# Optimization experiments

Hardware: AMD Instinct MI355X
Metric: run time of the kernel (lower is better)

The kernel has to match this reference:

```python
import jax, jax.numpy as jnp
import numpy as np

N_NODES = 20000
N_EDGES = 320000
N_FEAT = 128
HID = 64
HEADS = 4
N_CLS = 16
NEG_SLOPE = 0.2


def setup_inputs() -> dict:
    key = jax.random.key(0)
    ks = jax.random.split(key, 12)
    x = jax.random.normal(ks[0], (N_NODES, N_FEAT), dtype=jnp.float32)
    edge_index = jax.random.randint(ks[1], (2, N_EDGES), 0, N_NODES, dtype=jnp.int64)
    # layer 1: GATConv(128 -> 64, heads=4, concat)
    s1 = 1.0 / np.sqrt(N_FEAT)
    W1 = jax.random.uniform(ks[2], (N_FEAT, HEADS * HID), jnp.float32, -s1, s1)
    a_src1 = jax.random.uniform(ks[3], (HEADS, HID), jnp.float32, -s1, s1)
    a_dst1 = jax.random.uniform(ks[4], (HEADS, HID), jnp.float32, -s1, s1)
    b1 = jnp.zeros((HEADS * HID,), jnp.float32)
    # layer 2: GATConv(256 -> 16, heads=1)
    s2 = 1.0 / np.sqrt(HEADS * HID)
    W2 = jax.random.uniform(ks[5], (HEADS * HID, N_CLS), jnp.float32, -s2, s2)
    a_src2 = jax.random.uniform(ks[6], (1, N_CLS), jnp.float32, -s2, s2)
    a_dst2 = jax.random.uniform(ks[7], (1, N_CLS), jnp.float32, -s2, s2)
    b2 = jnp.zeros((N_CLS,), jnp.float32)
    return {"x": x, "edge_index": edge_index, "W1": W1, "a_src1": a_src1,
            "a_dst1": a_dst1, "b1": b1, "W2": W2, "a_src2": a_src2,
            "a_dst2": a_dst2, "b2": b2}


def gat_conv(x, src, dst, W, a_src, a_dst, bias, n_nodes):
    # x: [N, F_in]; W: [F_in, H*C]; a_src/a_dst: [H, C]
    H, C = a_src.shape
    h = (x @ W).reshape(n_nodes, H, C)                     # [N, H, C]
    al_src = jnp.sum(h * a_src[None], axis=-1)             # [N, H]
    al_dst = jnp.sum(h * a_dst[None], axis=-1)             # [N, H]
    e = jax.nn.leaky_relu(al_src[src] + al_dst[dst], NEG_SLOPE)  # [E, H]
    # segment softmax over incoming edges of each destination node
    m = jax.ops.segment_max(e, dst, num_segments=n_nodes)  # [N, H]
    e = jnp.exp(e - m[dst])
    denom = jax.ops.segment_sum(e, dst, num_segments=n_nodes)
    alpha = e / (denom[dst] + 1e-16)                       # [E, H]
    msg = h[src] * alpha[:, :, None]                       # [E, H, C]
    out = jax.ops.segment_sum(msg, dst, num_segments=n_nodes)  # [N, H, C]
    return out.reshape(n_nodes, H * C) + bias


def reference(x, edge_index, W1, a_src1, a_dst1, b1, W2, a_src2, a_dst2, b2):
    n = x.shape[0]
    loops = jnp.arange(n, dtype=edge_index.dtype)
    src = jnp.concatenate([edge_index[0], loops])
    dst = jnp.concatenate([edge_index[1], loops])
    # eval mode: dropout is identity
    h = jax.nn.elu(gat_conv(x, src, dst, W1, a_src1, a_dst1, b1, n))
    out = gat_conv(h, src, dst, W2, a_src2, a_dst2, b2, n)
    return out
```

## Files before the change

### kernel.cpp

```cpp
#include <hip/hip_runtime.h>
#include <hip/hip_bf16.h>
#include <hip/hip_fp16.h>
#include <math.h>

#define N_NODES 20000
#define N_EDGES 320000
#define E_TOT   (N_EDGES + N_NODES)
#define N_FEAT  128
#define NEG_SLOPE 0.2f
#define MAXDEG  96

typedef _Float16 half8 __attribute__((ext_vector_type(8)));
typedef float f32x4 __attribute__((ext_vector_type(4)));

__global__ void k_zero(int* __restrict__ cur){
  int i = blockIdx.x * blockDim.x + threadIdx.x;
  if (i < N_NODES) cur[i] = 0;
}

__global__ void k_pre(const int* __restrict__ ei, int* __restrict__ cur,
                      int* __restrict__ adjS,
                      const float* __restrict__ x, _Float16* __restrict__ xh,
                      const float* __restrict__ W1, _Float16* __restrict__ W1t){
  int tid = blockIdx.x * blockDim.x + threadIdx.x;
  if (tid < E_TOT){
    int s, d;
    if (tid < N_EDGES){ s = ei[tid]; d = ei[N_EDGES + tid]; }
    else              { s = d = tid - N_EDGES; }
    int pos = atomicAdd(&cur[d], 1);
    if (pos < MAXDEG) adjS[d * MAXDEG + pos] = s;
  }
  if (tid < (N_NODES * N_FEAT / 8)){
    float4 a = *(const float4*)&x[(size_t)tid * 8];
    float4 b = *(const float4*)&x[(size_t)tid * 8 + 4];
    union { __half2 h2[4]; half8 h8; } u;
    u.h2[0] = __floats2half2_rn(a.x, a.y);
    u.h2[1] = __floats2half2_rn(a.z, a.w);
    u.h2[2] = __floats2half2_rn(b.x, b.y);
    u.h2[3] = __floats2half2_rn(b.z, b.w);
    *(half8*)&xh[(size_t)tid * 8] = u.h8;
  }
  int u2 = tid - (N_NODES * N_FEAT / 8);
  if (u2 >= 0 && u2 < 4096){
    int n = u2 >> 4, ks = u2 & 15;
    union { __half2 h2[4]; half8 h8; } u;
    float v[8];
    #pragma unroll
    for (int r = 0; r < 8; ++r) v[r] = W1[(size_t)(ks * 8 + r) * 256 + n];
    u.h2[0] = __floats2half2_rn(v[0], v[1]);
    u.h2[1] = __floats2half2_rn(v[2], v[3]);
    u.h2[2] = __floats2half2_rn(v[4], v[5]);
    u.h2[3] = __floats2half2_rn(v[6], v[7]);
    *(half8*)&W1t[(size_t)n * 128 + ks * 8] = u.h8;
  }
}

__global__ __launch_bounds__(256) void k_gemm1(
                        const _Float16* __restrict__ xh, const _Float16* __restrict__ W1t,
                        const float* __restrict__ as1, const float* __restrict__ ad1,
                        _Float16* __restrict__ h1h,
                        float* __restrict__ alS, float* __restrict__ alD){
  __shared__ _Float16 xt[64][136];
  __shared__ _Float16 Wt[64][136];
  int t  = threadIdx.x;
  int m0 = blockIdx.x * 64;
  int by = blockIdx.y;
  int j0 = by * 64;
  #pragma unroll
  for (int ii = 0; ii < 4; ++ii){
    int f = t + ii * 256;
    int r = f >> 4, s = f & 15;
    half8 xv = (half8)(_Float16)0.f;
    if (m0 + r < N_NODES) xv = *(const half8*)&xh[(size_t)(m0 + r) * 128 + s * 8];
    *(half8*)&xt[r][s * 8] = xv;
    half8 wv = *(const half8*)&W1t[(size_t)(j0 + r) * 128 + s * 8];
    *(half8*)&Wt[r][s * 8] = wv;
  }
  __syncthreads();

  int w = t >> 6, lane = t & 63;
  int g = lane >> 4, mi = lane & 15;
  f32x4 acc[4] = {};
  #pragma unroll
  for (int kk = 0; kk < 4; ++kk){
    int ko = kk * 32 + g * 8;
    half8 b = *(const half8*)&xt[w * 16 + mi][ko];
    #pragma unroll
    for (int s = 0; s < 4; ++s){
      half8 a = *(const half8*)&Wt[s * 16 + mi][ko];
      acc[s] = __builtin_amdgcn_mfma_f32_16x16x32_f16(a, b, acc[s], 0, 0, 0);
    }
  }

  int m = m0 + w * 16 + mi;
  float s_ = 0.f, d_ = 0.f;
  #pragma unroll
  for (int s = 0; s < 4; ++s){
    int nb = j0 + s * 16 + g * 4;
    float4 asv = *(const float4*)&as1[nb];
    float4 adv = *(const float4*)&ad1[nb];
    s_ += acc[s][0] * asv.x + acc[s][1] * asv.y + acc[s][2] * asv.z + acc[s][3] * asv.w;
    d_ += acc[s][0] * adv.x + acc[s][1] * adv.y + acc[s][2] * adv.z + acc[s][3] * adv.w;
    if (m < N_NODES){
      union { __half2 h2[2]; float2 f2; } u;
      u.h2[0] = __floats2half2_rn(acc[s][0], acc[s][1]);
      u.h2[1] = __floats2half2_rn(acc[s][2], acc[s][3]);
      *(float2*)&h1h[(size_t)m * 256 + nb] = u.f2;
    }
  }
  s_ += __shfl_xor(s_, 16); s_ += __shfl_xor(s_, 32);
  d_ += __shfl_xor(d_, 16); d_ += __shfl_xor(d_, 32);
  if (g == 0 && m < N_NODES){ alS[m * 4 + by] = s_; alD[m * 4 + by] = d_; }
}

__global__ __launch_bounds__(256) void k_attn1(
                        const int* __restrict__ cur, const int* __restrict__ adjS,
                        const __half* __restrict__ h1h,
                        const float* __restrict__ alS, const float* __restrict__ alD,
                        const float* __restrict__ b1, _Float16* __restrict__ heluh){
  int b    = blockIdx.x;
  int slot = b & 7;
  int h    = slot & 3;
  int g    = (slot >> 2) * 625 + (b >> 3);
  int t    = threadIdx.x;
  int w    = t >> 6, lane = t & 63;
  int grp  = lane >> 4, l16 = lane & 15;
  int n    = g * 16 + w * 4 + grp;

  int cnt  = cur[n]; cnt = (cnt > MAXDEG) ? MAXDEG : cnt;
  int start = n * MAXDEG, end = start + cnt;
  float ald = alD[n * 4 + h];
  const __half* __restrict__ hb = h1h + h * 64 + l16 * 4;

  float4 A0 = make_float4(0.f,0.f,0.f,0.f), A1 = A0, A2 = A0, A3 = A0;
  float d0 = 0.f, d1 = 0.f, d2 = 0.f, d3 = 0.f;
  int i = start;
  for (; i + 3 < end; i += 4){
    int s0 = adjS[i],     s1 = adjS[i + 1];
    int s2 = adjS[i + 2], s3 = adjS[i + 3];
    float t0 = alS[s0 * 4 + h] + ald;
    float t1 = alS[s1 * 4 + h] + ald;
    float t2 = alS[s2 * 4 + h] + ald;
    float t3 = alS[s3 * 4 + h] + ald;
    t0 = (t0 > 0.f) ? t0 : NEG_SLOPE * t0;
    t1 = (t1 > 0.f) ? t1 : NEG_SLOPE * t1;
    t2 = (t2 > 0.f) ? t2 : NEG_SLOPE * t2;
    t3 = (t3 > 0.f) ? t3 : NEG_SLOPE * t3;
    float w0 = __expf(t0), w1 = __expf(t1), w2 = __expf(t2), w3 = __expf(t3);
    float2 r0 = *(const float2*)&hb[(size_t)s0 * 256];
    float2 r1 = *(const float2*)&hb[(size_t)s1 * 256];
    float2 r2 = *(const float2*)&hb[(size_t)s2 * 256];
    float2 r3 = *(const float2*)&hb[(size_t)s3 * 256];
    const __half2* p0 = (const __half2*)&r0;
    const __half2* p1 = (const __half2*)&r1;
    const __half2* p2 = (const __half2*)&r2;
    const __half2* p3 = (const __half2*)&r3;
    float2 v0a = __half22float2(p0[0]), v0b = __half22float2(p0[1]);
    float2 v1a = __half22float2(p1[0]), v1b = __half22float2(p1[1]);
    float2 v2a = __half22float2(p2[0]), v2b = __half22float2(p2[1]);
    float2 v3a = __half22float2(p3[0]), v3b = __half22float2(p3[1]);
    A0.x += w0 * v0a.x; A0.y += w0 * v0a.y; A0.z += w0 * v0b.x; A0.w += w0 * v0b.y;
    A1.x += w1 * v1a.x; A1.y += w1 * v1a.y; A1.z += w1 * v1b.x; A1.w += w1 * v1b.y;
    A2.x += w2 * v2a.x; A2.y += w2 * v2a.y; A2.z += w2 * v2b.x; A2.w += w2 * v2b.y;
    A3.x += w3 * v3a.x; A3.y += w3 * v3a.y; A3.z += w3 * v3b.x; A3.w += w3 * v3b.y;
    d0 += w0; d1 += w1; d2 += w2; d3 += w3;
  }
  for (; i < end; ++i){
    int s0 = adjS[i];
    float t0 = alS[s0 * 4 + h] + ald;
    t0 = (t0 > 0.f) ? t0 : NEG_SLOPE * t0;
    float w0 = __expf(t0);
    float2 r0 = *(const float2*)&hb[(size_t)s0 * 256];
    const __half2* p0 = (const __half2*)&r0;
    float2 v0a = __half22float2(p0[0]), v0b = __half22float2(p0[1]);
    A0.x += w0 * v0a.x; A0.y += w0 * v0a.y; A0.z += w0 * v0b.x; A0.w += w0 * v0b.y;
    d0 += w0;
  }
  float rinv = 1.f / (((d0 + d1) + (d2 + d3)) + 1e-16f);
  float4 bv = *(const float4*)&b1[h * 64 + l16 * 4];
  float4 o;
  o.x = ((A0.x + A1.x) + (A2.x + A3.x)) * rinv + bv.x;
  o.y = ((A0.y + A1.y) + (A2.y + A3.y)) * rinv + bv.y;
  o.z = ((A0.z + A1.z) + (A2.z + A3.z)) * rinv + bv.z;
  o.w = ((A0.w + A1.w) + (A2.w + A3.w)) * rinv + bv.w;
  o.x = (o.x > 0.f) ? o.x : (__expf(o.x) - 1.f);
  o.y = (o.y > 0.f) ? o.y : (__expf(o.y) - 1.f);
  o.z = (o.z > 0.f) ? o.z : (__expf(o.z) - 1.f);
  o.w = (o.w > 0.f) ? o.w : (__expf(o.w) - 1.f);
  union { __half2 h2[2]; float2 f2; } u;
  u.h2[0] = __floats2half2_rn(o.x, o.y);
  u.h2[1] = __floats2half2_rn(o.z, o.w);
  *(float2*)&heluh[(size_t)n * 256 + h * 64 + l16 * 4] = u.f2;
}

__global__ __launch_bounds__(256) void k_gemm2(
                        const _Float16* __restrict__ heluh, const float* __restrict__ W2,
                        const float* __restrict__ as2, const float* __restrict__ ad2,
                        float* __restrict__ h2, float* __restrict__ alS, float* __restrict__ alD){
  __shared__ _Float16 Ht[64][264];
  __shared__ _Float16 Wt[16][264];
  int t = threadIdx.x;
  int n0 = blockIdx.x * 64;
  #pragma unroll
  for (int ii = 0; ii < 8; ++ii){
    int f = t + ii * 256;
    int r = f >> 5, s = f & 31;
    half8 v = (half8)(_Float16)0.f;
    if (n0 + r < N_NODES) v = *(const half8*)&heluh[(size_t)(n0 + r) * 256 + s * 8];
    *(half8*)&Ht[r][s * 8] = v;
  }
  {
    int k = t;
    float4 w0 = *(const float4*)&W2[k * 16 + 0];
    float4 w1 = *(const float4*)&W2[k * 16 + 4];
    float4 w2 = *(const float4*)&W2[k * 16 + 8];
    float4 w3 = *(const float4*)&W2[k * 16 + 12];
    float wv[16] = {w0.x,w0.y,w0.z,w0.w, w1.x,w1.y,w1.z,w1.w,
                    w2.x,w2.y,w2.z,w2.w, w3.x,w3.y,w3.z,w3.w};
    #pragma unroll
    for (int c = 0; c < 16; ++c) Wt[c][k] = (_Float16)wv[c];
  }
  __syncthreads();

  int w = t >> 6, lane = t & 63;
  int g = lane >> 4, mi = lane & 15;
  f32x4 acc = {};
  #pragma unroll
  for (int kk = 0; kk < 8; ++kk){
    int ko = kk * 32 + g * 8;
    half8 b = *(const half8*)&Ht[w * 16 + mi][ko];
    half8 a = *(const half8*)&Wt[mi][ko];
    acc = __builtin_amdgcn_mfma_f32_16x16x32_f16(a, b, acc, 0, 0, 0);
  }
  int n = n0 + w * 16 + mi;
  float4 asv = *(const float4*)&as2[g * 4];
  float4 adv = *(const float4*)&ad2[g * 4];
  float s_ = acc[0] * asv.x + acc[1] * asv.y + acc[2] * asv.z + acc[3] * asv.w;
  float d_ = acc[0] * adv.x + acc[1] * adv.y + acc[2] * adv.z + acc[3] * adv.w;
  s_ += __shfl_xor(s_, 16); s_ += __shfl_xor(s_, 32);
  d_ += __shfl_xor(d_, 16); d_ += __shfl_xor(d_, 32);
  if (n < N_NODES){
    float4 hv = make_float4(acc[0], acc[1], acc[2], acc[3]);
    *(float4*)&h2[(size_t)n * 16 + g * 4] = hv;
    if (g == 0){ alS[n] = s_; alD[n] = d_; }
  }
}

__global__ __launch_bounds__(256) void k_attn2(
                        const int* __restrict__ cur, const int* __restrict__ adjS,
                        const float* __restrict__ h2,
                        const float* __restrict__ alS, const float* __restrict__ alD,
                        const float* __restrict__ b2, float* __restrict__ out){
  int t    = threadIdx.x;
  int w    = t >> 6, lane = t & 63;
  int grp  = lane >> 4, l16 = lane & 15;
  int j    = l16 >> 2, c4 = l16 & 3;
  int n    = blockIdx.x * 16 + w * 4 + grp;

  int cnt  = cur[n]; cnt = (cnt > MAXDEG) ? MAXDEG : cnt;
  int start = n * MAXDEG, end = start + cnt;
  float ald = alD[n];
  float4 acc = make_float4(0.f,0.f,0.f,0.f);
  float den = 0.f;
  for (int i = start + j; i < end; i += 4){
    int s = adjS[i];
    float tt = alS[s] + ald;
    tt = (tt > 0.f) ? tt : NEG_SLOPE * tt;
    float wv = __expf(tt);
    float4 v = *(const float4*)&h2[(size_t)s * 16 + c4 * 4];
    acc.x += wv * v.x; acc.y += wv * v.y; acc.z += wv * v.z; acc.w += wv * v.w;
    den += wv;
  }
  #pragma unroll
  for (int off = 4; off <= 8; off <<= 1){
    acc.x += __shfl_xor(acc.x, off);
    acc.y += __shfl_xor(acc.y, off);
    acc.z += __shfl_xor(acc.z, off);
    acc.w += __shfl_xor(acc.w, off);
    den   += __shfl_xor(den, off);
  }
  if (j == 0){
    float rinv = 1.f / (den + 1e-16f);
    float4 bv = *(const float4*)&b2[c4 * 4];
    float4 o;
    o.x = acc.x * rinv + bv.x; o.y = acc.y * rinv + bv.y;
    o.z = acc.z * rinv + bv.z; o.w = acc.w * rinv + bv.w;
    *(float4*)&out[(size_t)n * 16 + c4 * 4] = o;
  }
}

extern "C" void kernel_launch(void* const* d_in, const int* in_sizes, int n_in,
                              void* d_out, int out_size, void* d_ws, size_t ws_size,
                              hipStream_t stream){
  const float* x   = (const float*)d_in[0];
  const int*   ei  = (const int*)d_in[1];
  const float* W1  = (const float*)d_in[2];
  const float* as1 = (const float*)d_in[3];
  const float* ad1 = (const float*)d_in[4];
  const float* b1  = (const float*)d_in[5];
  const float* W2  = (const float*)d_in[6];
  const float* as2 = (const float*)d_in[7];
  const float* ad2 = (const float*)d_in[8];
  const float* b2  = (const float*)d_in[9];
  float* out = (float*)d_out;

  float* fws = (float*)d_ws;
  size_t off = 0;
  __half* h1h = (__half*)(fws + off); off += (size_t)N_NODES * 128;
  _Float16* xh  = (_Float16*)(fws + off); off += (size_t)N_NODES * 64;
  _Float16* W1t = (_Float16*)(fws + off); off += 256 * 64;
  _Float16* heluh = (_Float16*)(fws + off); off += (size_t)N_NODES * 128;
  float* h2   = fws + off; off += (size_t)N_NODES * 16;
  float* alS1 = fws + off; off += N_NODES * 4;
  float* alD1 = fws + off; off += N_NODES * 4;
  float* alS2 = fws + off; off += N_NODES;
  float* alD2 = fws + off; off += N_NODES;
  int* cur  = (int*)(fws + off); off += N_NODES;
  int* adjS = (int*)(fws + off); off += (size_t)N_NODES * MAXDEG;

  const int XW = N_NODES * N_FEAT / 8 + 4096;
  const int PRE_N = (E_TOT > XW ? E_TOT : XW);

  k_zero<<<(N_NODES + 255) / 256, 256, 0, stream>>>(cur);
  k_pre<<<(PRE_N + 255) / 256, 256, 0, stream>>>(ei, cur, adjS, x, xh, W1, W1t);
  k_gemm1<<<dim3(313, 4), 256, 0, stream>>>(xh, W1t, as1, ad1, (_Float16*)h1h, alS1, alD1);
  k_attn1<<<5000, 256, 0, stream>>>(cur, adjS, h1h, alS1, alD1, b1, heluh);
  k_gemm2<<<313, 256, 0, stream>>>(heluh, W2, as2, ad2, h2, alS2, alD2);
  k_attn2<<<1250, 256, 0, stream>>>(cur, adjS, h2, alS2, alD2, b2, out);
}
```

Baseline: 91.12 us.

## Fuse adjacency build into GEMM1 and merge zero/convert kernels; prefetch adjacency as int4

Counter zeroing now happens inside the x/W1 fp16 conversion kernel, which removes one launch. The edge-bucketing pass with its atomics moves from the preprocessing kernel into the first GEMM kernel as a grid-stride loop, so the scattered atomic work overlaps with GEMM tile loads. The layer-1 attention loop now loads neighbour indices as int4 vectors and fetches the next group ahead of use. The atomic scatter work is now spread over fewer threads, which adds latency at the front of each GEMM block. The int4 loads depend on the 16-byte alignment that MAXDEG=96 provides.

Result: faster. 80.15 us (-12.0%).

```diff
diff --git a/kernel.cpp b/kernel.cpp
--- a/kernel.cpp
+++ b/kernel.cpp
@@ -13,23 +13,11 @@
 typedef _Float16 half8 __attribute__((ext_vector_type(8)));
 typedef float f32x4 __attribute__((ext_vector_type(4)));
 
-__global__ void k_zero(int* __restrict__ cur){
-  int i = blockIdx.x * blockDim.x + threadIdx.x;
-  if (i < N_NODES) cur[i] = 0;
-}
-
-__global__ void k_pre(const int* __restrict__ ei, int* __restrict__ cur,
-                      int* __restrict__ adjS,
-                      const float* __restrict__ x, _Float16* __restrict__ xh,
-                      const float* __restrict__ W1, _Float16* __restrict__ W1t){
+__global__ void k_init(int* __restrict__ cur,
+                       const float* __restrict__ x, _Float16* __restrict__ xh,
+                       const float* __restrict__ W1, _Float16* __restrict__ W1t){
   int tid = blockIdx.x * blockDim.x + threadIdx.x;
-  if (tid < E_TOT){
-    int s, d;
-    if (tid < N_EDGES){ s = ei[tid]; d = ei[N_EDGES + tid]; }
-    else              { s = d = tid - N_EDGES; }
-    int pos = atomicAdd(&cur[d], 1);
-    if (pos < MAXDEG) adjS[d * MAXDEG + pos] = s;
-  }
+  if (tid < N_NODES) cur[tid] = 0;
   if (tid < (N_NODES * N_FEAT / 8)){
     float4 a = *(const float4*)&x[(size_t)tid * 8];
     float4 b = *(const float4*)&x[(size_t)tid * 8 + 4];
@@ -40,9 +28,8 @@
     u.h2[3] = __floats2half2_rn(b.z, b.w);
     *(half8*)&xh[(size_t)tid * 8] = u.h8;
   }
-  int u2 = tid - (N_NODES * N_FEAT / 8);
-  if (u2 >= 0 && u2 < 4096){
-    int n = u2 >> 4, ks = u2 & 15;
+  if (tid < 4096){
+    int n = tid >> 4, ks = tid & 15;
     union { __half2 h2[4]; half8 h8; } u;
     float v[8];
     #pragma unroll
@@ -59,10 +46,26 @@
                         const _Float16* __restrict__ xh, const _Float16* __restrict__ W1t,
                         const float* __restrict__ as1, const float* __restrict__ ad1,
                         _Float16* __restrict__ h1h,
-                        float* __restrict__ alS, float* __restrict__ alD){
+                        float* __restrict__ alS, float* __restrict__ alD,
+                        const int* __restrict__ ei, int* __restrict__ cur,
+                        int* __restrict__ adjS){
   __shared__ _Float16 xt[64][136];
   __shared__ _Float16 Wt[64][136];
   int t  = threadIdx.x;
+
+  {
+    int fb = blockIdx.y * 313 + blockIdx.x;
+    int gtid = fb * 256 + t;
+    const int GSZ = 313 * 4 * 256;
+    for (int e = gtid; e < E_TOT; e += GSZ){
+      int s, d;
+      if (e < N_EDGES){ s = ei[e]; d = ei[N_EDGES + e]; }
+      else            { s = d = e - N_EDGES; }
+      int pos = atomicAdd(&cur[d], 1);
+      if (pos < MAXDEG) adjS[d * MAXDEG + pos] = s;
+    }
+  }
+
   int m0 = blockIdx.x * 64;
   int by = blockIdx.y;
   int j0 = by * 64;
@@ -135,35 +138,40 @@
   float4 A0 = make_float4(0.f,0.f,0.f,0.f), A1 = A0, A2 = A0, A3 = A0;
   float d0 = 0.f, d1 = 0.f, d2 = 0.f, d3 = 0.f;
   int i = start;
-  for (; i + 3 < end; i += 4){
-    int s0 = adjS[i],     s1 = adjS[i + 1];
-    int s2 = adjS[i + 2], s3 = adjS[i + 3];
-    float t0 = alS[s0 * 4 + h] + ald;
-    float t1 = alS[s1 * 4 + h] + ald;
-    float t2 = alS[s2 * 4 + h] + ald;
-    float t3 = alS[s3 * 4 + h] + ald;
-    t0 = (t0 > 0.f) ? t0 : NEG_SLOPE * t0;
-    t1 = (t1 > 0.f) ? t1 : NEG_SLOPE * t1;
-    t2 = (t2 > 0.f) ? t2 : NEG_SLOPE * t2;
-    t3 = (t3 > 0.f) ? t3 : NEG_SLOPE * t3;
-    float w0 = __expf(t0), w1 = __expf(t1), w2 = __expf(t2), w3 = __expf(t3);
-    float2 r0 = *(const float2*)&hb[(size_t)s0 * 256];
-    float2 r1 = *(const float2*)&hb[(size_t)s1 * 256];
-    float2 r2 = *(const float2*)&hb[(size_t)s2 * 256];
-    float2 r3 = *(const float2*)&hb[(size_t)s3 * 256];
-    const __half2* p0 = (const __half2*)&r0;
-    const __half2* p1 = (const __half2*)&r1;
-    const __half2* p2 = (const __half2*)&r2;
-    const __half2* p3 = (const __half2*)&r3;
-    float2 v0a = __half22float2(p0[0]), v0b = __half22float2(p0[1]);
-    float2 v1a = __half22float2(p1[0]), v1b = __half22float2(p1[1]);
-    float2 v2a = __half22float2(p2[0]), v2b = __half22float2(p2[1]);
-    float2 v3a = __half22float2(p3[0]), v3b = __half22float2(p3[1]);
-    A0.x += w0 * v0a.x; A0.y += w0 * v0a.y; A0.z += w0 * v0b.x; A0.w += w0 * v0b.y;
-    A1.x += w1 * v1a.x; A1.y += w1 * v1a.y; A1.z += w1 * v1b.x; A1.w += w1 * v1b.y;
-    A2.x += w2 * v2a.x; A2.y += w2 * v2a.y; A2.z += w2 * v2b.x; A2.w += w2 * v2b.y;
-    A3.x += w3 * v3a.x; A3.y += w3 * v3a.y; A3.z += w3 * v3b.x; A3.w += w3 * v3b.y;
-    d0 += w0; d1 += w1; d2 += w2; d3 += w3;
+  if (i + 3 < end){
+    int4 q = *(const int4*)&adjS[i];
+    while (i + 3 < end){
+      int s0 = q.x, s1 = q.y, s2 = q.z, s3 = q.w;
+      int inext = i + 4;
+      if (inext + 3 < end) q = *(const int4*)&adjS[inext];
+      float t0 = alS[s0 * 4 + h] + ald;
+      float t1 = alS[s1 * 4 + h] + ald;
+      float t2 = alS[s2 * 4 + h] + ald;
+      float t3 = alS[s3 * 4 + h] + ald;
+      t0 = (t0 > 0.f) ? t0 : NEG_SLOPE * t0;
+      t1 = (t1 > 0.f) ? t1 : NEG_SLOPE * t1;
+      t2 = (t2 > 0.f) ? t2 : NEG_SLOPE * t2;
+      t3 = (t3 > 0.f) ? t3 : NEG_SLOPE * t3;
+      float w0 = __expf(t0), w1 = __expf(t1), w2 = __expf(t2), w3 = __expf(t3);
+      float2 r0 = *(const float2*)&hb[(size_t)s0 * 256];
+      float2 r1 = *(const float2*)&hb[(size_t)s1 * 256];
+      float2 r2 = *(const float2*)&hb[(size_t)s2 * 256];
+      float2 r3 = *(const float2*)&hb[(size_t)s3 * 256];
+      const __half2* p0 = (const __half2*)&r0;
+      const __half2* p1 = (const __half2*)&r1;
+      const __half2* p2 = (const __half2*)&r2;
+      const __half2* p3 = (const __half2*)&r3;
+      float2 v0a = __half22float2(p0[0]), v0b = __half22float2(p0[1]);
+      float2 v1a = __half22float2(p1[0]), v1b = __half22float2(p1[1]);
+      float2 v2a = __half22float2(p2[0]), v2b = __half22float2(p2[1]);
+      float2 v3a = __half22float2(p3[0]), v3b = __half22float2(p3[1]);
+      A0.x += w0 * v0a.x; A0.y += w0 * v0a.y; A0.z += w0 * v0b.x; A0.w += w0 * v0b.y;
+      A1.x += w1 * v1a.x; A1.y += w1 * v1a.y; A1.z += w1 * v1b.x; A1.w += w1 * v1b.y;
+      A2.x += w2 * v2a.x; A2.y += w2 * v2a.y; A2.z += w2 * v2b.x; A2.w += w2 * v2b.y;
+      A3.x += w3 * v3a.x; A3.y += w3 * v3a.y; A3.z += w3 * v3b.x; A3.w += w3 * v3b.y;
+      d0 += w0; d1 += w1; d2 += w2; d3 += w3;
+      i = inext;
+    }
   }
   for (; i < end; ++i){
     int s0 = adjS[i];
@@ -318,12 +326,9 @@
   int* cur  = (int*)(fws + off); off += N_NODES;
   int* adjS = (int*)(fws + off); off += (size_t)N_NODES * MAXDEG;
 
-  const int XW = N_NODES * N_FEAT / 8 + 4096;
-  const int PRE_N = (E_TOT > XW ? E_TOT : XW);
-
-  k_zero<<<(N_NODES + 255) / 256, 256, 0, stream>>>(cur);
-  k_pre<<<(PRE_N + 255) / 256, 256, 0, stream>>>(ei, cur, adjS, x, xh, W1, W1t);
-  k_gemm1<<<dim3(313, 4), 256, 0, stream>>>(xh, W1t, as1, ad1, (_Float16*)h1h, alS1, alD1);
+  k_init<<<(N_NODES * N_FEAT / 8 + 255) / 256, 256, 0, stream>>>(cur, x, xh, W1, W1t);
+  k_gemm1<<<dim3(313, 4), 256, 0, stream>>>(xh, W1t, as1, ad1, (_Float16*)h1h,
+                                            alS1, alD1, ei, cur, adjS);
   k_attn1<<<5000, 256, 0, stream>>>(cur, adjS, h1h, alS1, alD1, b1, heluh);
   k_gemm2<<<313, 256, 0, stream>>>(heluh, W2, as2, ad2, h2, alS2, alD2);
   k_attn2<<<1250, 256, 0, stream>>>(cur, adjS, h2, alS2, alD2, b2, out);
```
